# Performance work log

Hardware: AMD Instinct MI355X
Metric: run time of the kernel (lower is better)

Reference implementation:

```python
import jax, jax.numpy as jnp
import numpy as np

CH_IN = 64
CH_OUT = 64
KSIZE = 2
DILATION = 1
HID = 32


def _conv1x1(z, w, b):
    # z: [B, Cin, K], w: [Cout, Cin], b: [Cout] -> [B, Cout, K]
    return jnp.einsum('oi,bik->bok', w, z) + b[None, :, None]


def setup_inputs() -> dict:
    key = jax.random.key(0)
    ks = jax.random.split(key, 10)
    B, T, K, ZDIM = 8, 65536, 1024, 128
    s = 0.05
    return {
        'x': jax.random.normal(ks[0], (B, CH_IN, T), jnp.float32),
        'z': jax.random.normal(ks[1], (B, ZDIM, K), jnp.float32),
        'w1': jax.random.normal(ks[2], (HID, ZDIM), jnp.float32) * s,
        'b1': jax.random.normal(ks[3], (HID,), jnp.float32) * s,
        'w2': jax.random.normal(ks[4], (CH_IN * CH_OUT * KSIZE, HID), jnp.float32) * s,
        'b2': jax.random.normal(ks[5], (CH_IN * CH_OUT * KSIZE,), jnp.float32) * s,
        'w3': jax.random.normal(ks[6], (HID, ZDIM), jnp.float32) * s,
        'b3': jax.random.normal(ks[7], (HID,), jnp.float32) * s,
        'w4': jax.random.normal(ks[8], (CH_OUT, HID), jnp.float32) * s,
        'b4': jax.random.normal(ks[9], (CH_OUT,), jnp.float32) * s,
    }


def reference(x, z, w1, b1, w2, b2, w3, b3, w4, b4):
    B, _, T = x.shape
    K = z.shape[-1]
    S = T // K  # samples per conditioning step
    pad = DILATION * (KSIZE - 1)
    xp = jnp.pad(x, ((0, 0), (0, 0), (pad, 0)))
    # unfold: concat shifted copies along channel dim -> [B, CH_IN*KSIZE, T]
    xu = jnp.concatenate(
        [xp[:, :, pad - i * DILATION: pad - i * DILATION + T] for i in range(KSIZE)],
        axis=1)
    # [B*K, S, CH_IN*KSIZE]
    xr = xu.transpose(0, 2, 1).reshape(B * K, S, CH_IN * KSIZE)
    # hyper-generated weights: [B, CH_IN*KSIZE*CH_OUT, K]
    wfeat = _conv1x1(jax.nn.relu(_conv1x1(z, w1, b1)), w2, b2)
    weight = wfeat.reshape(B, CH_IN * KSIZE, CH_OUT, K).transpose(0, 3, 1, 2)
    weight = weight.reshape(B * K, CH_IN * KSIZE, CH_OUT)
    # hyper-generated bias: [B*K, CH_OUT]
    bfeat = _conv1x1(jax.nn.relu(_conv1x1(z, w3, b3)), w4, b4)  # [B, CH_OUT, K]
    bias = bfeat.transpose(0, 2, 1).reshape(B * K, CH_OUT)
    # batched matmul + bias
    y = jnp.einsum('nsc,nco->nso', xr, weight) + bias[:, None, :]
    return y.reshape(B, T, CH_OUT).transpose(0, 2, 1)
```

## Files before the change

### kernel.cpp

```cpp
#include <hip/hip_runtime.h>

#define CIN   64
#define COUT  64
#define HID   32
#define ZD    128
#define KC    1024
#define SPC   64
#define TLEN  65536

typedef __attribute__((ext_vector_type(8))) short bf16x8;
typedef __attribute__((ext_vector_type(4))) float f32x4;

__device__ __forceinline__ unsigned f2bf(float f) {
    unsigned u = __float_as_uint(f);
    unsigned r = u + 0x7fffu + ((u >> 16) & 1u);
    return r >> 16;
}
__device__ __forceinline__ unsigned pk2(float a, float b) {
    return f2bf(a) | (f2bf(b) << 16);
}

__global__ void cast_w2_kernel(const float* __restrict__ w2, unsigned* __restrict__ w2b) {
    int i  = blockIdx.x * 256 + threadIdx.x;
    int r  = i >> 4;
    int hp = i & 15;
    w2b[i] = pk2(w2[r * HID + 2 * hp], w2[r * HID + 2 * hp + 1]);
}

__global__ __launch_bounds__(256)
void transpose_cast_x(const float* __restrict__ x, unsigned short* __restrict__ xT) {
    __shared__ unsigned short s[64][66];
    const int blk  = blockIdx.x;
    const int b    = blk >> 10;
    const int t0   = (blk & 1023) << 6;
    const int lane = threadIdx.x & 63;
    const int wv   = threadIdx.x >> 6;
    const float* xb = x + (size_t)b * CIN * TLEN;
    #pragma unroll
    for (int cc = 0; cc < 16; ++cc) {
        int c = cc * 4 + wv;
        s[lane][c] = (unsigned short)f2bf(xb[(size_t)c * TLEN + t0 + lane]);
    }
    __syncthreads();
    unsigned short* ob = xT + ((size_t)b * TLEN + t0) * CIN;
    #pragma unroll
    for (int half = 0; half < 2; ++half) {
        int si = (half * 256 + threadIdx.x) * 8;
        int t = si >> 6, c = si & 63;
        const unsigned* sp = (const unsigned*)&s[t][c];
        uint4 v; v.x = sp[0]; v.y = sp[1]; v.z = sp[2]; v.w = sp[3];
        *(uint4*)&ob[(size_t)t * CIN + c] = v;
    }
}

template<bool USE_XT>
__global__ __launch_bounds__(256, 2)
void hyperconv_mfma(const float* __restrict__ x, const unsigned short* __restrict__ xT,
                    const float* __restrict__ z,
                    const float* __restrict__ w1, const float* __restrict__ b1,
                    const float* __restrict__ b2,
                    const float* __restrict__ w3, const float* __restrict__ b3,
                    const float* __restrict__ w4, const float* __restrict__ b4,
                    const uint4* __restrict__ w2b,
                    float* __restrict__ out)
{
    __shared__ __align__(16) float s_z[4][ZD];
    __shared__ __align__(16) float s_h3[4][HID];
    __shared__ __align__(16) float s_bias[4][COUT];
    __shared__ __align__(16) short s_h1b[4][HID];
    __shared__ __align__(16) short s_wc[4][2048];

    const int tid  = threadIdx.x;
    const int w    = tid >> 6;
    const int lane = tid & 63;
    const int l15  = lane & 15;
    const int q    = lane >> 4;
    const int n0   = blockIdx.x * 4;
    const int b    = n0 >> 10;
    const int kk0  = n0 & 1023;

    #pragma unroll
    for (int i = 0; i < 2; ++i) {
        int idx = tid + i * 256;
        int g = idx >> 7, d = idx & 127;
        s_z[g][d] = z[((size_t)b * ZD + d) * KC + kk0 + g];
    }
    __syncthreads();

    {
        int g = tid >> 6, u = tid & 63;
        const float* wrow = (u < HID) ? (w1 + u * ZD) : (w3 + (u - HID) * ZD);
        float acc = (u < HID) ? b1[u] : b3[u - HID];
        #pragma unroll
        for (int d4 = 0; d4 < ZD / 4; ++d4) {
            float4 wv = *(const float4*)(wrow + 4 * d4);
            float4 zv = *(const float4*)(&s_z[g][4 * d4]);
            acc += wv.x * zv.x + wv.y * zv.y + wv.z * zv.z + wv.w * zv.w;
        }
        acc = fmaxf(acc, 0.f);
        if (u < HID) s_h1b[g][u] = (short)f2bf(acc);
        else         s_h3[g][u - HID] = acc;
    }
    __syncthreads();

    {
        int g = tid >> 6, o = tid & 63;
        float acc = b4[o];
        #pragma unroll
        for (int h4 = 0; h4 < HID / 4; ++h4) {
            float4 wv = *(const float4*)(w4 + o * HID + 4 * h4);
            float4 hv = *(const float4*)(&s_h3[g][4 * h4]);
            acc += wv.x * hv.x + wv.y * hv.y + wv.z * hv.z + wv.w * hv.w;
        }
        s_bias[g][o] = acc;
    }

    bf16x8 afrag = *(const bf16x8*)&s_h1b[l15 >> 2][q * 8];

    auto produce = [&](int ksr) {
        const int rb = ksr * 2048 + w * 512;
        #pragma unroll
        for (int ntl = 0; ntl < 4; ++ntl) {
            float cvq[8];
            #pragma unroll
            for (int jj = 0; jj < 8; ++jj) {
                int r = rb + 64 * jj + 16 * ntl + l15;
                float b2v = b2[r];
                bf16x8 bfrag = __builtin_bit_cast(bf16x8, w2b[r * 4 + q]);
                f32x4 c = __builtin_amdgcn_mfma_f32_16x16x32_bf16(
                    afrag, bfrag, (f32x4){b2v, b2v, b2v, b2v}, 0, 0, 0);
                cvq[jj] = c[0];
            }
            uint4 res;
            res.x = pk2(cvq[0], cvq[1]);
            res.y = pk2(cvq[2], cvq[3]);
            res.z = pk2(cvq[4], cvq[5]);
            res.w = pk2(cvq[6], cvq[7]);
            *(uint4*)&s_wc[q][w * 512 + (16 * ntl + l15) * 8] = res;
        }
    };

    produce(0);
    __syncthreads();

    const int t0 = (kk0 + w) * SPC;
    const float* xb = x + (size_t)b * CIN * TLEN;
    const unsigned short* xtb = xT + (size_t)b * TLEN * CIN;

    f32x4 acc[4][4];
    #pragma unroll
    for (int i = 0; i < 4; ++i)
        #pragma unroll
        for (int j = 0; j < 4; ++j) acc[i][j] = (f32x4){0.f, 0.f, 0.f, 0.f};

    #pragma unroll
    for (int ks = 0; ks < 4; ++ks) {
        const int koff = (ks >= 2) ? -1 : 0;
        const int c0 = (ks & 1) * 32 + 8 * q;
        bf16x8 bfr[4];
        if (USE_XT) {
            #pragma unroll
            for (int st = 0; st < 4; ++st) {
                int t = t0 + 16 * st + l15 + koff;
                uint4 p = (uint4){0u, 0u, 0u, 0u};
                if (t >= 0) p = *(const uint4*)&xtb[(size_t)t * CIN + c0];
                bfr[st] = __builtin_bit_cast(bf16x8, p);
            }
        } else {
            #pragma unroll
            for (int st = 0; st < 4; ++st) {
                int t = t0 + 16 * st + l15 + koff;
                int tc = t < 0 ? 0 : t;
                float v[8];
                #pragma unroll
                for (int j = 0; j < 8; ++j)
                    v[j] = xb[(size_t)(c0 + j) * TLEN + tc];
                if (t < 0) {
                    #pragma unroll
                    for (int j = 0; j < 8; ++j) v[j] = 0.f;
                }
                uint4 p;
                p.x = pk2(v[0], v[1]); p.y = pk2(v[2], v[3]);
                p.z = pk2(v[4], v[5]); p.w = pk2(v[6], v[7]);
                bfr[st] = __builtin_bit_cast(bf16x8, p);
            }
        }

        #pragma unroll
        for (int ot = 0; ot < 4; ++ot) {
            bf16x8 afr = *(const bf16x8*)&s_wc[w][q * 512 + (16 * ot + l15) * 8];
            #pragma unroll
            for (int st = 0; st < 4; ++st)
                acc[ot][st] = __builtin_amdgcn_mfma_f32_16x16x32_bf16(
                    afr, bfr[st], acc[ot][st], 0, 0, 0);
        }

        if (ks < 3) {
            __syncthreads();
            produce(ks + 1);
            __syncthreads();
        }
    }

    float* ob = out + (size_t)b * COUT * TLEN;
    #pragma unroll
    for (int ot = 0; ot < 4; ++ot) {
        f32x4 bv = *(const f32x4*)&s_bias[w][16 * ot + 4 * q];
        #pragma unroll
        for (int st = 0; st < 4; ++st) {
            int t = t0 + 16 * st + l15;
            #pragma unroll
            for (int reg = 0; reg < 4; ++reg)
                ob[(size_t)(16 * ot + 4 * q + reg) * TLEN + t] = acc[ot][st][reg] + bv[reg];
        }
    }
}

extern "C" void kernel_launch(void* const* d_in, const int* in_sizes, int n_in,
                              void* d_out, int out_size, void* d_ws, size_t ws_size,
                              hipStream_t stream) {
    const float* x  = (const float*)d_in[0];
    const float* z  = (const float*)d_in[1];
    const float* w1 = (const float*)d_in[2];
    const float* b1 = (const float*)d_in[3];
    const float* w2 = (const float*)d_in[4];
    const float* b2 = (const float*)d_in[5];
    const float* w3 = (const float*)d_in[6];
    const float* b3 = (const float*)d_in[7];
    const float* w4 = (const float*)d_in[8];
    const float* b4 = (const float*)d_in[9];
    float* out = (float*)d_out;

    unsigned* w2b = (unsigned*)d_ws;
    unsigned short* xT = (unsigned short*)((char*)d_ws + 524288);
    const size_t need_xt = 524288ull + (size_t)8 * TLEN * CIN * 2;

    cast_w2_kernel<<<512, 256, 0, stream>>>(w2, w2b);
    if (ws_size >= need_xt) {
        transpose_cast_x<<<8192, 256, 0, stream>>>(x, xT);
        hyperconv_mfma<true><<<2048, 256, 0, stream>>>(x, xT, z, w1, b1, b2, w3, b3, w4, b4,
                                                       (const uint4*)w2b, out);
    } else {
        hyperconv_mfma<false><<<2048, 256, 0, stream>>>(x, xT, z, w1, b1, b2, w3, b3, w4, b4,
                                                        (const uint4*)w2b, out);
    }
}
```

Before: 378.5 us.

## Split fused hyperconv into separate weight-generation and apply kernels via workspace

```diff
diff --git a/kernel.cpp b/kernel.cpp
--- a/kernel.cpp
+++ b/kernel.cpp
@@ -52,6 +52,158 @@
         *(uint4*)&ob[(size_t)t * CIN + c] = v;
     }
 }
+
+
+__global__ __launch_bounds__(256, 4)
+void wgen_kernel(const float* __restrict__ z,
+                 const float* __restrict__ w1, const float* __restrict__ b1,
+                 const float* __restrict__ b2,
+                 const float* __restrict__ w3, const float* __restrict__ b3,
+                 const float* __restrict__ w4, const float* __restrict__ b4,
+                 const uint4* __restrict__ w2b,
+                 unsigned short* __restrict__ Wg, float* __restrict__ biasg)
+{
+    __shared__ __align__(16) float s_z[4][ZD];
+    __shared__ __align__(16) float s_h3[4][HID];
+    __shared__ __align__(16) short s_h1b[4][HID];
+
+    const int tid  = threadIdx.x;
+    const int w    = tid >> 6;
+    const int lane = tid & 63;
+    const int l15  = lane & 15;
+    const int q    = lane >> 4;
+    const int n0   = blockIdx.x * 4;
+    const int b    = n0 >> 10;
+    const int kk0  = n0 & 1023;
+
+    #pragma unroll
+    for (int i = 0; i < 2; ++i) {
+        int idx = tid + i * 256;
+        int g = idx >> 7, d = idx & 127;
+        s_z[g][d] = z[((size_t)b * ZD + d) * KC + kk0 + g];
+    }
+    __syncthreads();
+
+    {
+        int g = tid >> 6, u = tid & 63;
+        const float* wrow = (u < HID) ? (w1 + u * ZD) : (w3 + (u - HID) * ZD);
+        float acc = (u < HID) ? b1[u] : b3[u - HID];
+        #pragma unroll
+        for (int d4 = 0; d4 < ZD / 4; ++d4) {
+            float4 wv = *(const float4*)(wrow + 4 * d4);
+            float4 zv = *(const float4*)(&s_z[g][4 * d4]);
+            acc += wv.x * zv.x + wv.y * zv.y + wv.z * zv.z + wv.w * zv.w;
+        }
+        acc = fmaxf(acc, 0.f);
+        if (u < HID) s_h1b[g][u] = (short)f2bf(acc);
+        else         s_h3[g][u - HID] = acc;
+    }
+    __syncthreads();
+
+    {
+        int g = tid >> 6, o = tid & 63;
+        float acc = b4[o];
+        #pragma unroll
+        for (int h4 = 0; h4 < HID / 4; ++h4) {
+            float4 wv = *(const float4*)(w4 + o * HID + 4 * h4);
+            float4 hv = *(const float4*)(&s_h3[g][4 * h4]);
+            acc += wv.x * hv.x + wv.y * hv.y + wv.z * hv.z + wv.w * hv.w;
+        }
+        biasg[(size_t)(n0 + g) * COUT + o] = acc;
+    }
+
+    bf16x8 afrag = *(const bf16x8*)&s_h1b[l15 >> 2][q * 8];
+    unsigned short* Wq = Wg + (size_t)(n0 + q) * 8192;
+
+    #pragma unroll
+    for (int ksr = 0; ksr < 4; ++ksr) {
+        const int rb = ksr * 2048 + w * 512;
+        #pragma unroll
+        for (int ntl = 0; ntl < 4; ++ntl) {
+            float cvq[8];
+            #pragma unroll
+            for (int jj = 0; jj < 8; ++jj) {
+                int r = rb + 64 * jj + 16 * ntl + l15;
+                float b2v = b2[r];
+                bf16x8 bfrag = __builtin_bit_cast(bf16x8, w2b[r * 4 + q]);
+                f32x4 c = __builtin_amdgcn_mfma_f32_16x16x32_bf16(
+                    afrag, bfrag, (f32x4){b2v, b2v, b2v, b2v}, 0, 0, 0);
+                cvq[jj] = c[0];
+            }
+            uint4 res;
+            res.x = pk2(cvq[0], cvq[1]);
+            res.y = pk2(cvq[2], cvq[3]);
+            res.z = pk2(cvq[4], cvq[5]);
+            res.w = pk2(cvq[6], cvq[7]);
+            *(uint4*)&Wq[rb + (16 * ntl + l15) * 8] = res;
+        }
+    }
+}
+
+__global__ __launch_bounds__(256, 5)
+void hyperconv_apply(const unsigned short* __restrict__ xT,
+                     const unsigned short* __restrict__ Wg,
+                     const float* __restrict__ biasg,
+                     float* __restrict__ out)
+{
+    const int tid  = threadIdx.x;
+    const int w    = tid >> 6;
+    const int lane = tid & 63;
+    const int l15  = lane & 15;
+    const int q    = lane >> 4;
+    const int smp  = blockIdx.x * 2 + (w >> 1);
+    const int oh   = w & 1;
+    const int b    = smp >> 10;
+    const int t0   = (smp & 1023) * SPC;
+
+    const unsigned short* xtb = xT + (size_t)b * TLEN * CIN;
+    const unsigned short* Wn  = Wg + (size_t)smp * 8192;
+
+    f32x4 acc[2][4];
+    #pragma unroll
+    for (int i = 0; i < 2; ++i)
+        #pragma unroll
+        for (int j = 0; j < 4; ++j) acc[i][j] = (f32x4){0.f, 0.f, 0.f, 0.f};
+
+    #pragma unroll
+    for (int ks = 0; ks < 4; ++ks) {
+        const int koff = (ks >= 2) ? -1 : 0;
+        const int c0   = (ks & 1) * 32 + 8 * q;
+        bf16x8 bfr[4];
+        #pragma unroll
+        for (int st = 0; st < 4; ++st) {
+            int t = t0 + 16 * st + l15 + koff;
+            uint4 p = (uint4){0u, 0u, 0u, 0u};
+            if (t >= 0) p = *(const uint4*)&xtb[(size_t)t * CIN + c0];
+            bfr[st] = __builtin_bit_cast(bf16x8, p);
+        }
+        #pragma unroll
+        for (int ot = 0; ot < 2; ++ot) {
+            const int ot2 = oh * 2 + ot;
+            bf16x8 afr = *(const bf16x8*)&Wn[ks * 2048 + q * 512 + (16 * ot2 + l15) * 8];
+            #pragma unroll
+            for (int st = 0; st < 4; ++st)
+                acc[ot][st] = __builtin_amdgcn_mfma_f32_16x16x32_bf16(
+                    afr, bfr[st], acc[ot][st], 0, 0, 0);
+        }
+    }
+
+    const float* bn = biasg + (size_t)smp * COUT;
+    float* ob = out + (size_t)b * COUT * TLEN;
+    #pragma unroll
+    for (int ot = 0; ot < 2; ++ot) {
+        const int ot2 = oh * 2 + ot;
+        f32x4 bv = *(const f32x4*)&bn[16 * ot2 + 4 * q];
+        #pragma unroll
+        for (int st = 0; st < 4; ++st) {
+            int t = t0 + 16 * st + l15;
+            #pragma unroll
+            for (int reg = 0; reg < 4; ++reg)
+                ob[(size_t)(16 * ot2 + 4 * q + reg) * TLEN + t] = acc[ot][st][reg] + bv[reg];
+        }
+    }
+}
+
 
 template<bool USE_XT>
 __global__ __launch_bounds__(256, 2)
@@ -231,12 +383,24 @@
     const float* b4 = (const float*)d_in[9];
     float* out = (float*)d_out;
 
-    unsigned* w2b = (unsigned*)d_ws;
-    unsigned short* xT = (unsigned short*)((char*)d_ws + 524288);
-    const size_t need_xt = 524288ull + (size_t)8 * TLEN * CIN * 2;
+    const size_t off_xt   = 524288;
+    const size_t off_wg   = off_xt + 67108864;
+    const size_t off_bias = off_wg + 134217728;
+    const size_t need_xt   = off_wg;
+    const size_t need_full = off_bias + 2097152;
+
+    unsigned* w2b       = (unsigned*)d_ws;
+    unsigned short* xT  = (unsigned short*)((char*)d_ws + off_xt);
+    unsigned short* Wg  = (unsigned short*)((char*)d_ws + off_wg);
+    float* biasg        = (float*)((char*)d_ws + off_bias);
 
     cast_w2_kernel<<<512, 256, 0, stream>>>(w2, w2b);
-    if (ws_size >= need_xt) {
+    if (ws_size >= need_full) {
+        transpose_cast_x<<<8192, 256, 0, stream>>>(x, xT);
+        wgen_kernel<<<2048, 256, 0, stream>>>(z, w1, b1, b2, w3, b3, w4, b4,
+                                              (const uint4*)w2b, Wg, biasg);
+        hyperconv_apply<<<4096, 256, 0, stream>>>(xT, Wg, biasg, out);
+    } else if (ws_size >= need_xt) {
         transpose_cast_x<<<8192, 256, 0, stream>>>(x, xT);
         hyperconv_mfma<true><<<2048, 256, 0, stream>>>(x, xT, z, w1, b1, b2, w3, b3, w4, b4,
                                                        (const uint4*)w2b, out);
```

Result: slower. 455.5 us (+20.3%).
